# Optimization experiments

Measured on AMD Instinct MI355X. Metric: run time of the kernel, lower is better.

Reference implementation:

```python
import jax, jax.numpy as jnp
import numpy as np

B, S, D, H = 4, 1024, 1024, 16
DK = D // H


def _rel_shift(x):
    # Transformer-XL relative shift: x is (b, h, t1, t2) with t1 == t2
    b, h, t1, t2 = x.shape
    x = jnp.pad(x, ((0, 0), (0, 0), (0, 0), (1, 0)))  # pad left of last dim
    x = x.reshape(b, h, t2 + 1, t1)
    return x[:, :, 1:, :].reshape(b, h, t1, t2)


def setup_inputs() -> dict:
    rng = jax.random.key(0)
    ks = jax.random.split(rng, 10)
    w = 0.02
    return {
        "query": jax.random.normal(ks[0], (B, S, D), jnp.float32),
        "key": jax.random.normal(ks[1], (B, S, D), jnp.float32),
        "value": jax.random.normal(ks[2], (B, S, D), jnp.float32),
        "mask": jnp.ones((B, S), dtype=bool),
        "Wq": jax.random.normal(ks[3], (D, D), jnp.float32) * w,
        "Wk": jax.random.normal(ks[4], (D, D), jnp.float32) * w,
        "Wv": jax.random.normal(ks[5], (D, D), jnp.float32) * w,
        "Wp": jax.random.normal(ks[6], (D, D), jnp.float32) * w,
        "Wo": jax.random.normal(ks[7], (D, D), jnp.float32) * w,
        "pos_bias_u": jax.random.normal(ks[8], (H, DK), jnp.float32) * w,
        "pos_bias_v": jax.random.normal(ks[9], (H, DK), jnp.float32) * w,
    }


def reference(query, key, value, mask, Wq, Wk, Wv, Wp, Wo, pos_bias_u, pos_bias_v):
    b, s, dm = query.shape
    h, dk = pos_bias_u.shape

    # sinusoidal relative position embeddings (positions s-1 ... 0)
    inv_freq = 1.0 / (10000.0 ** (jnp.arange(0, dm, 2, dtype=jnp.float32) / dm))
    pos_seq = jnp.arange(s - 1, -1, -1, dtype=jnp.float32)
    sin_inp = pos_seq[:, None] * inv_freq[None, :]              # (s, dm/2)
    pos_emb = jnp.concatenate([jnp.sin(sin_inp), jnp.cos(sin_inp)], -1)  # (s, dm)

    # projections (torch Linear: y = x @ W.T)
    q = (query @ Wq.T).reshape(b, s, h, dk).transpose(0, 2, 1, 3)  # (b,h,s,dk)
    k = (key @ Wk.T).reshape(b, s, h, dk).transpose(0, 2, 1, 3)
    v = (value @ Wv.T).reshape(b, s, h, dk).transpose(0, 2, 1, 3)
    p = (pos_emb @ Wp.T).reshape(s, h, dk).transpose(1, 0, 2)       # (h,s,dk), same for all batches

    content_score = jnp.einsum('bhqd,bhkd->bhqk', q + pos_bias_u[None, :, None, :], k)
    pos_score = jnp.einsum('bhqd,hkd->bhqk', q + pos_bias_v[None, :, None, :], p)
    pos_score = _rel_shift(pos_score)

    scores = (content_score + pos_score) / jnp.sqrt(jnp.float32(dk))
    attn_mask = mask[:, None, :, None] & mask[:, None, None, :]    # (b,1,q,k)
    scores = jnp.where(attn_mask, scores, jnp.float32(-1e9))

    attn = jax.nn.softmax(scores, axis=-1)  # dropout is identity at eval
    context = jnp.einsum('bhqk,bhkd->bqhd', attn, v).reshape(b, s, dm)
    return context @ Wo.T
```

## Files before the change

### kernel.cpp

```cpp
#include <hip/hip_runtime.h>
#include <math.h>

#define BATCH 4
#define SEQ   1024
#define DM    1024
#define NH    16
#define DK    64

typedef __attribute__((ext_vector_type(8))) short short8;
typedef __attribute__((ext_vector_type(4))) float f32x4;

__device__ inline unsigned short f2bf(float f) {
    unsigned u = __float_as_uint(f);
    unsigned r = (u + 0x7fffu + ((u >> 16) & 1u)) >> 16;
    return (unsigned short)r;
}
__device__ inline float bf2f(unsigned short s) {
    return __uint_as_float(((unsigned)s) << 16);
}
__device__ inline void split1(float x, unsigned short& h, unsigned short& l) {
    h = f2bf(x);
    l = f2bf(x - bf2f(h));
}

__global__ __launch_bounds__(256) void cvt_split(const float4* __restrict__ x,
                                                 ushort4* __restrict__ h,
                                                 ushort4* __restrict__ l, int n4) {
    int i = blockIdx.x * blockDim.x + threadIdx.x;
    if (i >= n4) return;
    float4 v = x[i];
    ushort4 hv, lv;
    split1(v.x, hv.x, lv.x);
    split1(v.y, hv.y, lv.y);
    split1(v.z, hv.z, lv.z);
    split1(v.w, hv.w, lv.w);
    h[i] = hv;
    l[i] = lv;
}

__global__ void posemb_kernel(float* __restrict__ pos_emb) {
    int idx = blockIdx.x * blockDim.x + threadIdx.x;
    if (idx >= SEQ * DM) return;
    int j = idx / DM, d = idx % DM;
    double pos = (double)(SEQ - 1 - j);
    int i = (d < DM / 2) ? d : d - DM / 2;
    double inv_freq = exp(-((2.0 * (double)i) / (double)DM) * log(10000.0));
    double a = pos * inv_freq;
    pos_emb[idx] = (d < DM / 2) ? (float)sin(a) : (float)cos(a);
}

__global__ __launch_bounds__(256) void prep_q(const float4* __restrict__ qp4,
                                              const float4* __restrict__ ub4,
                                              const float4* __restrict__ vb4,
                                              ushort4* __restrict__ quh,
                                              ushort4* __restrict__ qul,
                                              ushort4* __restrict__ qvh,
                                              ushort4* __restrict__ qvl) {
    int i = blockIdx.x * 256 + threadIdx.x;
    float4 q = qp4[i];
    int dm4 = i & (DM / 4 - 1);
    float4 u = ub4[dm4], v = vb4[dm4];
    ushort4 h, l;
    split1(q.x + u.x, h.x, l.x);
    split1(q.y + u.y, h.y, l.y);
    split1(q.z + u.z, h.z, l.z);
    split1(q.w + u.w, h.w, l.w);
    quh[i] = h; qul[i] = l;
    split1(q.x + v.x, h.x, l.x);
    split1(q.y + v.y, h.y, l.y);
    split1(q.z + v.z, h.z, l.z);
    split1(q.w + v.w, h.w, l.w);
    qvh[i] = h; qvl[i] = l;
}

__global__ __launch_bounds__(256) void vtrans_kernel(const float* __restrict__ vp,
                                                     unsigned short* __restrict__ vth,
                                                     unsigned short* __restrict__ vtl) {
    __shared__ float tile[64][65];
    int s0 = blockIdx.x * 64, h = blockIdx.y, b = blockIdx.z;
    int t = threadIdx.x;
#pragma unroll
    for (int i = 0; i < 16; i++) {
        int idx = t + 256 * i;
        int sl = idx >> 6, d = idx & 63;
        tile[sl][d] = vp[((size_t)b * SEQ + s0 + sl) * DM + h * DK + d];
    }
    __syncthreads();
    int bh = b * NH + h;
#pragma unroll
    for (int i = 0; i < 16; i++) {
        int idx = t + 256 * i;
        int dl = idx >> 6, sl = idx & 63;
        float x = tile[sl][dl];
        unsigned short hi, lo;
        split1(x, hi, lo);
        size_t o = ((size_t)bh * DK + dl) * SEQ + s0 + sl;
        vth[o] = hi;
        vtl[o] = lo;
    }
}

__device__ inline void load16(const void* g, void* l) {
    __builtin_amdgcn_global_load_lds(
        (const __attribute__((address_space(1))) unsigned int*)g,
        (__attribute__((address_space(3))) unsigned int*)l, 16, 0, 0);
}

__global__ __launch_bounds__(256) void gemm_split_nt(
        const unsigned short* __restrict__ Ah, const unsigned short* __restrict__ Al,
        const unsigned short* __restrict__ Bh, const unsigned short* __restrict__ Bl,
        float* __restrict__ C, int M, int N, int K,
        long aStride, long bStride, long cStride) {
    __shared__ __attribute__((aligned(16))) short Ah_s[128 * 32];
    __shared__ __attribute__((aligned(16))) short Al_s[128 * 32];
    __shared__ __attribute__((aligned(16))) short Bh_s[128 * 32];
    __shared__ __attribute__((aligned(16))) short Bl_s[128 * 32];

    int z = blockIdx.z;
    Ah += (size_t)z * aStride; Al += (size_t)z * aStride;
    Bh += (size_t)z * bStride; Bl += (size_t)z * bStride;
    C  += (size_t)z * cStride;

    int tid = threadIdx.x, w = tid >> 6, lane = tid & 63;
    int bm = blockIdx.y * 128, bn = blockIdx.x * 128;
    int quad = lane >> 4, tl = lane & 15;
    int wm = (w >> 1) * 64, wn = (w & 1) * 64;

    int sr = w * 32 + (lane >> 2);
    int sc = (lane & 3) * 8;
    const unsigned short* gA0h = Ah + (size_t)(bm + sr) * K + sc;
    const unsigned short* gA1h = Ah + (size_t)(bm + sr + 16) * K + sc;
    const unsigned short* gA0l = Al + (size_t)(bm + sr) * K + sc;
    const unsigned short* gA1l = Al + (size_t)(bm + sr + 16) * K + sc;
    const unsigned short* gB0h = Bh + (size_t)(bn + sr) * K + sc;
    const unsigned short* gB1h = Bh + (size_t)(bn + sr + 16) * K + sc;
    const unsigned short* gB0l = Bl + (size_t)(bn + sr) * K + sc;
    const unsigned short* gB1l = Bl + (size_t)(bn + sr + 16) * K + sc;
    short* lA0h = Ah_s + (w * 32) * 32;  short* lA1h = lA0h + 16 * 32;
    short* lA0l = Al_s + (w * 32) * 32;  short* lA1l = lA0l + 16 * 32;
    short* lB0h = Bh_s + (w * 32) * 32;  short* lB1h = lB0h + 16 * 32;
    short* lB0l = Bl_s + (w * 32) * 32;  short* lB1l = lB0l + 16 * 32;

    f32x4 acc[4][4];
#pragma unroll
    for (int mi = 0; mi < 4; mi++)
#pragma unroll
        for (int ni = 0; ni < 4; ni++)
            acc[mi][ni] = (f32x4){0.f, 0.f, 0.f, 0.f};

    for (int k0 = 0; k0 < K; k0 += 32) {
        load16(gA0h, lA0h); load16(gA1h, lA1h);
        load16(gA0l, lA0l); load16(gA1l, lA1l);
        load16(gB0h, lB0h); load16(gB1h, lB1h);
        load16(gB0l, lB0l); load16(gB1l, lB1l);
        gA0h += 32; gA1h += 32; gA0l += 32; gA1l += 32;
        gB0h += 32; gB1h += 32; gB0l += 32; gB1l += 32;
        __syncthreads();

        short8 ah[4], al[4], bh[4], bl[4];
#pragma unroll
        for (int mi = 0; mi < 4; mi++) {
            int r = wm + mi * 16 + tl;
            ah[mi] = *(const short8*)(Ah_s + r * 32 + quad * 8);
            al[mi] = *(const short8*)(Al_s + r * 32 + quad * 8);
        }
#pragma unroll
        for (int ni = 0; ni < 4; ni++) {
            int r = wn + ni * 16 + tl;
            bh[ni] = *(const short8*)(Bh_s + r * 32 + quad * 8);
            bl[ni] = *(const short8*)(Bl_s + r * 32 + quad * 8);
        }
#pragma unroll
        for (int mi = 0; mi < 4; mi++)
#pragma unroll
            for (int ni = 0; ni < 4; ni++) {
                acc[mi][ni] = __builtin_amdgcn_mfma_f32_16x16x32_bf16(
                    ah[mi], bh[ni], acc[mi][ni], 0, 0, 0);
                acc[mi][ni] = __builtin_amdgcn_mfma_f32_16x16x32_bf16(
                    al[mi], bh[ni], acc[mi][ni], 0, 0, 0);
                acc[mi][ni] = __builtin_amdgcn_mfma_f32_16x16x32_bf16(
                    ah[mi], bl[ni], acc[mi][ni], 0, 0, 0);
            }
        __syncthreads();
    }
#pragma unroll
    for (int mi = 0; mi < 4; mi++)
#pragma unroll
        for (int ni = 0; ni < 4; ni++)
#pragma unroll
            for (int r = 0; r < 4; r++)
                C[(size_t)(bm + wm + mi * 16 + quad * 4 + r) * N +
                  bn + wn + ni * 16 + tl] = acc[mi][ni][r];
}

__global__ __launch_bounds__(256) void gemm_scores(
        const unsigned short* __restrict__ quh, const unsigned short* __restrict__ qul,
        const unsigned short* __restrict__ qvh, const unsigned short* __restrict__ qvl,
        const unsigned short* __restrict__ kh,  const unsigned short* __restrict__ kl,
        const unsigned short* __restrict__ ph,  const unsigned short* __restrict__ pl,
        unsigned short* __restrict__ contC, unsigned short* __restrict__ posC,
        int bh0, int nc) {
    __shared__ __attribute__((aligned(16))) short Ah_s[128 * 32];
    __shared__ __attribute__((aligned(16))) short Al_s[128 * 32];
    __shared__ __attribute__((aligned(16))) short Bh_s[128 * 32];
    __shared__ __attribute__((aligned(16))) short Bl_s[128 * 32];

    int z = blockIdx.z;
    bool isPos = z >= nc;
    int zi = isPos ? z - nc : z;
    int bh = bh0 + zi, b = bh >> 4, h = bh & 15;
    size_t qoff = (size_t)b * SEQ * DM + h * DK;
    const unsigned short *Ah, *Al, *Bh, *Bl;
    if (!isPos) { Ah = quh + qoff; Al = qul + qoff; Bh = kh + qoff; Bl = kl + qoff; }
    else        { Ah = qvh + qoff; Al = qvl + qoff; Bh = ph + h * DK; Bl = pl + h * DK; }
    unsigned short* C = (isPos ? posC : contC) + (size_t)zi * SEQ * SEQ;

    int tid = threadIdx.x, w = tid >> 6, lane = tid & 63;
    int bm = blockIdx.y * 128, bn = blockIdx.x * 128;
    int quad = lane >> 4, tl = lane & 15;
    int wm = (w >> 1) * 64, wn = (w & 1) * 64;

    int sr = w * 32 + (lane >> 2);
    int sc = (lane & 3) * 8;
    const unsigned short* gA0h = Ah + (size_t)(bm + sr) * DM + sc;
    const unsigned short* gA1h = Ah + (size_t)(bm + sr + 16) * DM + sc;
    const unsigned short* gA0l = Al + (size_t)(bm + sr) * DM + sc;
    const unsigned short* gA1l = Al + (size_t)(bm + sr + 16) * DM + sc;
    const unsigned short* gB0h = Bh + (size_t)(bn + sr) * DM + sc;
    const unsigned short* gB1h = Bh + (size_t)(bn + sr + 16) * DM + sc;
    const unsigned short* gB0l = Bl + (size_t)(bn + sr) * DM + sc;
    const unsigned short* gB1l = Bl + (size_t)(bn + sr + 16) * DM + sc;
    short* lA0h = Ah_s + (w * 32) * 32;  short* lA1h = lA0h + 16 * 32;
    short* lA0l = Al_s + (w * 32) * 32;  short* lA1l = lA0l + 16 * 32;
    short* lB0h = Bh_s + (w * 32) * 32;  short* lB1h = lB0h + 16 * 32;
    short* lB0l = Bl_s + (w * 32) * 32;  short* lB1l = lB0l + 16 * 32;

    f32x4 acc[4][4];
#pragma unroll
    for (int mi = 0; mi < 4; mi++)
#pragma unroll
        for (int ni = 0; ni < 4; ni++)
            acc[mi][ni] = (f32x4){0.f, 0.f, 0.f, 0.f};

    for (int k0 = 0; k0 < DK; k0 += 32) {
        load16(gA0h, lA0h); load16(gA1h, lA1h);
        load16(gA0l, lA0l); load16(gA1l, lA1l);
        load16(gB0h, lB0h); load16(gB1h, lB1h);
        load16(gB0l, lB0l); load16(gB1l, lB1l);
        gA0h += 32; gA1h += 32; gA0l += 32; gA1l += 32;
        gB0h += 32; gB1h += 32; gB0l += 32; gB1l += 32;
        __syncthreads();

        short8 ah[4], al[4], bh[4], bl[4];
#pragma unroll
        for (int mi = 0; mi < 4; mi++) {
            int r = wm + mi * 16 + tl;
            ah[mi] = *(const short8*)(Ah_s + r * 32 + quad * 8);
            al[mi] = *(const short8*)(Al_s + r * 32 + quad * 8);
        }
#pragma unroll
        for (int ni = 0; ni < 4; ni++) {
            int r = wn + ni * 16 + tl;
            bh[ni] = *(const short8*)(Bh_s + r * 32 + quad * 8);
            bl[ni] = *(const short8*)(Bl_s + r * 32 + quad * 8);
        }
#pragma unroll
        for (int mi = 0; mi < 4; mi++)
#pragma unroll
            for (int ni = 0; ni < 4; ni++) {
                acc[mi][ni] = __builtin_amdgcn_mfma_f32_16x16x32_bf16(
                    ah[mi], bh[ni], acc[mi][ni], 0, 0, 0);
                acc[mi][ni] = __builtin_amdgcn_mfma_f32_16x16x32_bf16(
                    al[mi], bh[ni], acc[mi][ni], 0, 0, 0);
                acc[mi][ni] = __builtin_amdgcn_mfma_f32_16x16x32_bf16(
                    ah[mi], bl[ni], acc[mi][ni], 0, 0, 0);
            }
        __syncthreads();
    }
#pragma unroll
    for (int mi = 0; mi < 4; mi++)
#pragma unroll
        for (int ni = 0; ni < 4; ni++)
#pragma unroll
            for (int r = 0; r < 4; r++)
                C[(size_t)(bm + wm + mi * 16 + quad * 4 + r) * SEQ +
                  bn + wn + ni * 16 + tl] = f2bf(acc[mi][ni][r]);
}

__global__ __launch_bounds__(512) void content_softmax(
        const unsigned short* __restrict__ quh, const unsigned short* __restrict__ qul,
        const unsigned short* __restrict__ kh,  const unsigned short* __restrict__ kl,
        const unsigned short* __restrict__ posC, unsigned short* __restrict__ contC,
        int bh0) {
    __shared__ __attribute__((aligned(16))) short smem[69632];
    short* S_s = smem + 36864;

    int zi = blockIdx.y;
    int q0 = blockIdx.x * 32;
    int bh = bh0 + zi, b = bh >> 4, h = bh & 15;
    size_t qoff = (size_t)b * SEQ * DM + h * DK;
    const unsigned short* Ah = quh + qoff;
    const unsigned short* Al = qul + qoff;
    const unsigned short* Bh = kh + qoff;
    const unsigned short* Bl = kl + qoff;

    int t = threadIdx.x, w = t >> 6, lane = t & 63;
    int quad = lane >> 4, tl = lane & 15;
    int mi = w >> 2;
    int ni0 = (w & 3) * 2;

    {
        int r8 = w & 3;
        short* dst = smem + (w < 4 ? 0 : 2048) + r8 * 512;
        const unsigned short* srcb = (w < 4 ? Ah : Al);
        load16(srcb + (size_t)(q0 + r8 * 8 + (lane >> 3)) * DM + (lane & 7) * 8, dst);
    }
    {
        int bb = 4096;
#pragma unroll
        for (int i = 0; i < 2; i++) {
            int row = w * 16 + i * 8 + (lane >> 3);
            load16(Bh + (size_t)row * DM + (lane & 7) * 8, smem + bb + w * 1024 + i * 512);
            load16(Bl + (size_t)row * DM + (lane & 7) * 8, smem + bb + 8192 + w * 1024 + i * 512);
        }
    }
    __syncthreads();

    short8 afh[2], afl[2];
#pragma unroll
    for (int kc = 0; kc < 2; kc++) {
        afh[kc] = *(const short8*)(smem + (mi * 16 + tl) * 64 + kc * 32 + quad * 8);
        afl[kc] = *(const short8*)(smem + 2048 + (mi * 16 + tl) * 64 + kc * 32 + quad * 8);
    }

    for (int nb = 0; nb < 8; nb++) {
        int bb  = (nb & 1) ? 20480 : 4096;
        int nbb = (nb & 1) ? 4096 : 20480;
        if (nb < 7) {
            int n0 = (nb + 1) * 128;
#pragma unroll
            for (int i = 0; i < 2; i++) {
                int row = n0 + w * 16 + i * 8 + (lane >> 3);
                load16(Bh + (size_t)row * DM + (lane & 7) * 8, smem + nbb + w * 1024 + i * 512);
                load16(Bl + (size_t)row * DM + (lane & 7) * 8, smem + nbb + 8192 + w * 1024 + i * 512);
            }
        }

        f32x4 acc0 = (f32x4){0.f, 0.f, 0.f, 0.f};
        f32x4 acc1 = (f32x4){0.f, 0.f, 0.f, 0.f};
#pragma unroll
        for (int kc = 0; kc < 2; kc++) {
            short8 bh0f = *(const short8*)(smem + bb + ((ni0) * 16 + tl) * 64 + kc * 32 + quad * 8);
            short8 bl0f = *(const short8*)(smem + bb + 8192 + ((ni0) * 16 + tl) * 64 + kc * 32 + quad * 8);
            short8 bh1f = *(const short8*)(smem + bb + ((ni0 + 1) * 16 + tl) * 64 + kc * 32 + quad * 8);
            short8 bl1f = *(const short8*)(smem + bb + 8192 + ((ni0 + 1) * 16 + tl) * 64 + kc * 32 + quad * 8);
            acc0 = __builtin_amdgcn_mfma_f32_16x16x32_bf16(afh[kc], bh0f, acc0, 0, 0, 0);
            acc0 = __builtin_amdgcn_mfma_f32_16x16x32_bf16(afl[kc], bh0f, acc0, 0, 0, 0);
            acc0 = __builtin_amdgcn_mfma_f32_16x16x32_bf16(afh[kc], bl0f, acc0, 0, 0, 0);
            acc1 = __builtin_amdgcn_mfma_f32_16x16x32_bf16(afh[kc], bh1f, acc1, 0, 0, 0);
            acc1 = __builtin_amdgcn_mfma_f32_16x16x32_bf16(afl[kc], bh1f, acc1, 0, 0, 0);
            acc1 = __builtin_amdgcn_mfma_f32_16x16x32_bf16(afh[kc], bl1f, acc1, 0, 0, 0);
        }
#pragma unroll
        for (int r = 0; r < 4; r++) {
            int row = mi * 16 + quad * 4 + r;
            S_s[row * 1024 + nb * 128 + ni0 * 16 + tl]       = (short)f2bf(acc0[r]);
            S_s[row * 1024 + nb * 128 + (ni0 + 1) * 16 + tl] = (short)f2bf(acc1[r]);
        }
        __syncthreads();
    }

    int nrows = (q0 <= 991) ? 33 : 32;
    {
        float4* P4 = (float4*)smem;
        const float4* src4 = (const float4*)(posC + ((size_t)zi * SEQ + q0) * SEQ);
        int n4 = nrows * 128;
        for (int i = t; i < n4; i += 512) P4[i] = src4[i];
    }
    __syncthreads();

    const unsigned short* P_s = (const unsigned short*)smem;
#pragma unroll
    for (int j = 0; j < 4; j++) {
        int rl = w * 4 + j;
        int q = q0 + rl;
        const short* Srow = S_s + rl * 1024;
        float v[16];
        float m = -1e30f;
#pragma unroll
        for (int s = 0; s < 4; s++) {
            int kb = s * 256 + lane * 4;
            ushort4 sc = *(const ushort4*)(Srow + kb);
#pragma unroll
            for (int e = 0; e < 4; e++) {
                int k = kb + e;
                bool lo = (k <= q);
                int srow = rl + (lo ? 0 : 1);
                int scol = lo ? (k + SEQ - 1 - q) : (k - q - 2);
                float pos = 0.f;
                if (k != q + 1) pos = bf2f(P_s[srow * 1024 + scol]);
                float val = (bf2f(((const unsigned short*)&sc)[e]) + pos) * 0.125f;
                v[s * 4 + e] = val;
                m = fmaxf(m, val);
            }
        }
#pragma unroll
        for (int off = 32; off > 0; off >>= 1) m = fmaxf(m, __shfl_xor(m, off));
        float sum = 0.f;
#pragma unroll
        for (int i = 0; i < 16; i++) { v[i] = __expf(v[i] - m); sum += v[i]; }
#pragma unroll
        for (int off = 32; off > 0; off >>= 1) sum += __shfl_xor(sum, off);
        float inv = 1.0f / sum;
        unsigned short* crow = contC + ((size_t)zi * SEQ + q) * SEQ;
#pragma unroll
        for (int s = 0; s < 4; s++) {
            ushort4 o;
            o.x = f2bf(v[s * 4 + 0] * inv);
            o.y = f2bf(v[s * 4 + 1] * inv);
            o.z = f2bf(v[s * 4 + 2] * inv);
            o.w = f2bf(v[s * 4 + 3] * inv);
            *(ushort4*)(crow + s * 256 + lane * 4) = o;
        }
    }
}

__global__ __launch_bounds__(256) void gemm_pv(
        const unsigned short* __restrict__ probs,
        const unsigned short* __restrict__ vth, const unsigned short* __restrict__ vtl,
        unsigned short* __restrict__ cxh, unsigned short* __restrict__ cxl, int bh0) {
    __shared__ __attribute__((aligned(16))) short As[64 * 64];
    __shared__ __attribute__((aligned(16))) short Bhs[64 * 64];
    __shared__ __attribute__((aligned(16))) short Bls[64 * 64];

    int zi = blockIdx.z;
    int bh = bh0 + zi, b = bh >> 4, h = bh & 15;
    const unsigned short* A  = probs + (size_t)zi * SEQ * SEQ;
    const unsigned short* Bh = vth + (size_t)bh * DK * SEQ;
    const unsigned short* Bl = vtl + (size_t)bh * DK * SEQ;
    size_t coff = (size_t)b * SEQ * DM + h * DK;
    int bm = blockIdx.y * 64;

    int tid = threadIdx.x, w = tid >> 6, lane = tid & 63;
    int quad = lane >> 4, tl = lane & 15;
    int wm = (w >> 1) * 32, wn = (w & 1) * 32;

    int srow = w * 8 + (lane >> 3);
    int scol = (lane & 7) * 8;
    const unsigned short* gA  = A  + (size_t)(bm + srow) * SEQ + scol;
    const unsigned short* gBh = Bh + (size_t)srow * SEQ + scol;
    const unsigned short* gBl = Bl + (size_t)srow * SEQ + scol;

    f32x4 acc[2][2];
#pragma unroll
    for (int mi = 0; mi < 2; mi++)
#pragma unroll
        for (int ni = 0; ni < 2; ni++)
            acc[mi][ni] = (f32x4){0.f, 0.f, 0.f, 0.f};

    for (int k0 = 0; k0 < SEQ; k0 += 64) {
#pragma unroll
        for (int i = 0; i < 2; i++) {
            size_t go = (size_t)i * 32 * SEQ;
            load16(gA + go,  As  + i * 2048 + w * 512);
            load16(gBh + go, Bhs + i * 2048 + w * 512);
            load16(gBl + go, Bls + i * 2048 + w * 512);
        }
        gA += 64; gBh += 64; gBl += 64;
        __syncthreads();

#pragma unroll
        for (int kc = 0; kc < 2; kc++) {
            short8 a[2], bhf[2], blf[2];
#pragma unroll
            for (int mi = 0; mi < 2; mi++)
                a[mi] = *(const short8*)(As + (wm + mi * 16 + tl) * 64 + kc * 32 + quad * 8);
#pragma unroll
            for (int ni = 0; ni < 2; ni++) {
                bhf[ni] = *(const short8*)(Bhs + (wn + ni * 16 + tl) * 64 + kc * 32 + quad * 8);
                blf[ni] = *(const short8*)(Bls + (wn + ni * 16 + tl) * 64 + kc * 32 + quad * 8);
            }
#pragma unroll
            for (int mi = 0; mi < 2; mi++)
#pragma unroll
                for (int ni = 0; ni < 2; ni++) {
                    acc[mi][ni] = __builtin_amdgcn_mfma_f32_16x16x32_bf16(
                        a[mi], bhf[ni], acc[mi][ni], 0, 0, 0);
                    acc[mi][ni] = __builtin_amdgcn_mfma_f32_16x16x32_bf16(
                        a[mi], blf[ni], acc[mi][ni], 0, 0, 0);
                }
        }
        __syncthreads();
    }
#pragma unroll
    for (int mi = 0; mi < 2; mi++)
#pragma unroll
        for (int ni = 0; ni < 2; ni++)
#pragma unroll
            for (int r = 0; r < 4; r++) {
                size_t a = coff +
                    (size_t)(bm + wm + mi * 16 + quad * 4 + r) * DM +
                    wn + ni * 16 + tl;
                unsigned short hh, ll;
                split1(acc[mi][ni][r], hh, ll);
                cxh[a] = hh;
                cxl[a] = ll;
            }
}

extern "C" void kernel_launch(void* const* d_in, const int* in_sizes, int n_in,
                              void* d_out, int out_size, void* d_ws, size_t ws_size,
                              hipStream_t stream) {
    const float* query = (const float*)d_in[0];
    const float* key   = (const float*)d_in[1];
    const float* value = (const float*)d_in[2];
    const float* Wq = (const float*)d_in[4];
    const float* Wk = (const float*)d_in[5];
    const float* Wv = (const float*)d_in[6];
    const float* Wp = (const float*)d_in[7];
    const float* Wo = (const float*)d_in[8];
    const float* pu = (const float*)d_in[9];
    const float* pvb = (const float*)d_in[10];
    float* out = (float*)d_out;

    const size_t MB = 1u << 20;
    char* wsb = (char*)d_ws;
    float* posemb = (float*)(wsb + 0 * MB);
    float* pp     = (float*)(wsb + 4 * MB);
    float* qp     = (float*)(wsb + 8 * MB);
    float* kp     = (float*)(wsb + 24 * MB);
    float* vp     = (float*)(wsb + 40 * MB);
    unsigned short* qAh = (unsigned short*)(wsb + 56 * MB);
    unsigned short* qAl = (unsigned short*)(wsb + 64 * MB);
    unsigned short* kAh = (unsigned short*)(wsb + 72 * MB);
    unsigned short* kAl = (unsigned short*)(wsb + 80 * MB);
    unsigned short* vAh = (unsigned short*)(wsb + 88 * MB);
    unsigned short* vAl = (unsigned short*)(wsb + 96 * MB);
    unsigned short* Wqh = (unsigned short*)(wsb + 104 * MB);
    unsigned short* Wql = (unsigned short*)(wsb + 106 * MB);
    unsigned short* Wkh = (unsigned short*)(wsb + 108 * MB);
    unsigned short* Wkl = (unsigned short*)(wsb + 110 * MB);
    unsigned short* Wvh = (unsigned short*)(wsb + 112 * MB);
    unsigned short* Wvl = (unsigned short*)(wsb + 114 * MB);
    unsigned short* PEh = (unsigned short*)(wsb + 56 * MB);
    unsigned short* PEl = (unsigned short*)(wsb + 58 * MB);
    unsigned short* Wph = (unsigned short*)(wsb + 60 * MB);
    unsigned short* Wpl = (unsigned short*)(wsb + 62 * MB);
    unsigned short* quh = (unsigned short*)(wsb + 56 * MB);
    unsigned short* qul = (unsigned short*)(wsb + 64 * MB);
    unsigned short* qvh = (unsigned short*)(wsb + 72 * MB);
    unsigned short* qvl = (unsigned short*)(wsb + 80 * MB);
    unsigned short* khs = (unsigned short*)(wsb + 88 * MB);
    unsigned short* kls = (unsigned short*)(wsb + 96 * MB);
    unsigned short* phs = (unsigned short*)(wsb + 104 * MB);
    unsigned short* pls = (unsigned short*)(wsb + 106 * MB);
    unsigned short* vth = (unsigned short*)(wsb + 108 * MB);
    unsigned short* vtl = (unsigned short*)(wsb + 116 * MB);
    unsigned short* CXh = (unsigned short*)(wsb + 24 * MB);
    unsigned short* CXl = (unsigned short*)(wsb + 32 * MB);
    unsigned short* Woh = (unsigned short*)(wsb + 40 * MB);
    unsigned short* Wol = (unsigned short*)(wsb + 42 * MB);
    unsigned short* contC = (unsigned short*)(wsb + 124 * MB);

    int nc = (ws_size >= 252 * MB) ? 32 : 16;
    unsigned short* posC = contC + (size_t)nc * SEQ * SEQ;

    const int N4BIG = (BATCH * SEQ * DM) / 4;
    const int N4W   = (DM * DM) / 4;

    posemb_kernel<<<(SEQ * DM + 255) / 256, 256, 0, stream>>>(posemb);

    cvt_split<<<N4BIG / 256, 256, 0, stream>>>((const float4*)query, (ushort4*)qAh, (ushort4*)qAl, N4BIG);
    cvt_split<<<N4BIG / 256, 256, 0, stream>>>((const float4*)key,   (ushort4*)kAh, (ushort4*)kAl, N4BIG);
    cvt_split<<<N4BIG / 256, 256, 0, stream>>>((const float4*)value, (ushort4*)vAh, (ushort4*)vAl, N4BIG);
    cvt_split<<<N4W / 256, 256, 0, stream>>>((const float4*)Wq, (ushort4*)Wqh, (ushort4*)Wql, N4W);
    cvt_split<<<N4W / 256, 256, 0, stream>>>((const float4*)Wk, (ushort4*)Wkh, (ushort4*)Wkl, N4W);
    cvt_split<<<N4W / 256, 256, 0, stream>>>((const float4*)Wv, (ushort4*)Wvh, (ushort4*)Wvl, N4W);
    long aS = 8L * MB, bS = 2L * MB, cS = 4L * MB;
    gemm_split_nt<<<dim3(DM / 128, (BATCH * SEQ) / 128, 3), 256, 0, stream>>>(
        qAh, qAl, Wqh, Wql, qp, BATCH * SEQ, DM, DM, aS, bS, cS);

    cvt_split<<<(SEQ * DM / 4) / 256, 256, 0, stream>>>((const float4*)posemb, (ushort4*)PEh, (ushort4*)PEl, SEQ * DM / 4);
    cvt_split<<<N4W / 256, 256, 0, stream>>>((const float4*)Wp, (ushort4*)Wph, (ushort4*)Wpl, N4W);
    gemm_split_nt<<<dim3(DM / 128, SEQ / 128, 1), 256, 0, stream>>>(
        PEh, PEl, Wph, Wpl, pp, SEQ, DM, DM, 0, 0, 0);

    prep_q<<<N4BIG / 256, 256, 0, stream>>>((const float4*)qp, (const float4*)pu,
                                            (const float4*)pvb, (ushort4*)quh,
                                            (ushort4*)qul, (ushort4*)qvh, (ushort4*)qvl);
    cvt_split<<<N4BIG / 256, 256, 0, stream>>>((const float4*)kp, (ushort4*)khs, (ushort4*)kls, N4BIG);
    cvt_split<<<(SEQ * DM / 4) / 256, 256, 0, stream>>>((const float4*)pp, (ushort4*)phs, (ushort4*)pls, SEQ * DM / 4);
    vtrans_kernel<<<dim3(SEQ / 64, NH, BATCH), 256, 0, stream>>>(vp, vth, vtl);
    cvt_split<<<N4W / 256, 256, 0, stream>>>((const float4*)Wo, (ushort4*)Woh, (ushort4*)Wol, N4W);

    for (int c = 0; c < BATCH * NH; c += nc) {
        gemm_scores<<<dim3(SEQ / 128, SEQ / 128, nc), 256, 0, stream>>>(
            quh, qul, qvh, qvl, khs, kls, phs, pls, contC, posC, c, 0);
        content_softmax<<<dim3(SEQ / 32, nc), 512, 0, stream>>>(
            quh, qul, khs, kls, posC, contC, c);
        gemm_pv<<<dim3(1, SEQ / 64, nc), 256, 0, stream>>>(contC, vth, vtl,
                                                           CXh, CXl, c);
    }

    gemm_split_nt<<<dim3(DM / 128, (BATCH * SEQ) / 128, 1), 256, 0, stream>>>(
        CXh, CXl, Woh, Wol, out, BATCH * SEQ, DM, DM, 0, 0, 0);
}
```

Measured before the change: 607.5 us.

## Fuse PV matmul into softmax kernel and batch pos-proj GEMM with QKV

The softmax kernel now keeps normalized probabilities in shared memory (row stride padded to 1032) and multiplies them directly by V hi/lo fragments loaded from global. This removes the separate gemm_pv kernel and the round trip of the full probability matrix through global memory. The positional-embedding kernel now emits bf16 hi/lo splits directly, and the Wp projection runs as a fourth z-slice of the QKV GEMM launch, dropping a launch and a conversion pass. V is read from global without LDS staging in the fused loop, and each block redoes the V reads, which may add latency. Workspace layout is reshuffled and the contC buffer is removed.

```diff
diff --git a/kernel.cpp b/kernel.cpp
--- a/kernel.cpp
+++ b/kernel.cpp
@@ -38,7 +38,8 @@
     l[i] = lv;
 }
 
-__global__ void posemb_kernel(float* __restrict__ pos_emb) {
+__global__ void posemb_kernel(unsigned short* __restrict__ peh,
+                              unsigned short* __restrict__ pel) {
     int idx = blockIdx.x * blockDim.x + threadIdx.x;
     if (idx >= SEQ * DM) return;
     int j = idx / DM, d = idx % DM;
@@ -46,7 +47,11 @@
     int i = (d < DM / 2) ? d : d - DM / 2;
     double inv_freq = exp(-((2.0 * (double)i) / (double)DM) * log(10000.0));
     double a = pos * inv_freq;
-    pos_emb[idx] = (d < DM / 2) ? (float)sin(a) : (float)cos(a);
+    float v = (d < DM / 2) ? (float)sin(a) : (float)cos(a);
+    unsigned short hh, ll;
+    split1(v, hh, ll);
+    peh[idx] = hh;
+    pel[idx] = ll;
 }
 
 __global__ __launch_bounds__(256) void prep_q(const float4* __restrict__ qp4,
@@ -110,19 +115,27 @@
         const unsigned short* __restrict__ Ah, const unsigned short* __restrict__ Al,
         const unsigned short* __restrict__ Bh, const unsigned short* __restrict__ Bl,
         float* __restrict__ C, int M, int N, int K,
-        long aStride, long bStride, long cStride) {
+        long aStride, long bStride, long cStride,
+        const unsigned short* __restrict__ PEh, const unsigned short* __restrict__ PEl,
+        const unsigned short* __restrict__ Wph, const unsigned short* __restrict__ Wpl,
+        float* __restrict__ Cp) {
     __shared__ __attribute__((aligned(16))) short Ah_s[128 * 32];
     __shared__ __attribute__((aligned(16))) short Al_s[128 * 32];
     __shared__ __attribute__((aligned(16))) short Bh_s[128 * 32];
     __shared__ __attribute__((aligned(16))) short Bl_s[128 * 32];
 
     int z = blockIdx.z;
-    Ah += (size_t)z * aStride; Al += (size_t)z * aStride;
-    Bh += (size_t)z * bStride; Bl += (size_t)z * bStride;
-    C  += (size_t)z * cStride;
+    int bm = blockIdx.y * 128, bn = blockIdx.x * 128;
+    if (z == 3) {
+        if (bm >= SEQ) return;
+        Ah = PEh; Al = PEl; Bh = Wph; Bl = Wpl; C = Cp;
+    } else {
+        Ah += (size_t)z * aStride; Al += (size_t)z * aStride;
+        Bh += (size_t)z * bStride; Bl += (size_t)z * bStride;
+        C  += (size_t)z * cStride;
+    }
 
     int tid = threadIdx.x, w = tid >> 6, lane = tid & 63;
-    int bm = blockIdx.y * 128, bn = blockIdx.x * 128;
     int quad = lane >> 4, tl = lane & 15;
     int wm = (w >> 1) * 64, wn = (w & 1) * 64;
 
@@ -290,9 +303,11 @@
 __global__ __launch_bounds__(512) void content_softmax(
         const unsigned short* __restrict__ quh, const unsigned short* __restrict__ qul,
         const unsigned short* __restrict__ kh,  const unsigned short* __restrict__ kl,
-        const unsigned short* __restrict__ posC, unsigned short* __restrict__ contC,
+        const unsigned short* __restrict__ posC,
+        const unsigned short* __restrict__ vth, const unsigned short* __restrict__ vtl,
+        unsigned short* __restrict__ cxh, unsigned short* __restrict__ cxl,
         int bh0) {
-    __shared__ __attribute__((aligned(16))) short smem[69632];
+    __shared__ __attribute__((aligned(16))) short smem[69888];
     short* S_s = smem + 36864;
 
     int zi = blockIdx.y;
@@ -364,8 +379,8 @@
 #pragma unroll
         for (int r = 0; r < 4; r++) {
             int row = mi * 16 + quad * 4 + r;
-            S_s[row * 1024 + nb * 128 + ni0 * 16 + tl]       = (short)f2bf(acc0[r]);
-            S_s[row * 1024 + nb * 128 + (ni0 + 1) * 16 + tl] = (short)f2bf(acc1[r]);
+            S_s[row * 1032 + nb * 128 + ni0 * 16 + tl]       = (short)f2bf(acc0[r]);
+            S_s[row * 1032 + nb * 128 + (ni0 + 1) * 16 + tl] = (short)f2bf(acc1[r]);
         }
         __syncthreads();
     }
@@ -384,7 +399,7 @@
     for (int j = 0; j < 4; j++) {
         int rl = w * 4 + j;
         int q = q0 + rl;
-        const short* Srow = S_s + rl * 1024;
+        short* Srow = S_s + rl * 1032;
         float v[16];
         float m = -1e30f;
 #pragma unroll
@@ -412,7 +427,6 @@
 #pragma unroll
         for (int off = 32; off > 0; off >>= 1) sum += __shfl_xor(sum, off);
         float inv = 1.0f / sum;
-        unsigned short* crow = contC + ((size_t)zi * SEQ + q) * SEQ;
 #pragma unroll
         for (int s = 0; s < 4; s++) {
             ushort4 o;
@@ -420,92 +434,44 @@
             o.y = f2bf(v[s * 4 + 1] * inv);
             o.z = f2bf(v[s * 4 + 2] * inv);
             o.w = f2bf(v[s * 4 + 3] * inv);
-            *(ushort4*)(crow + s * 256 + lane * 4) = o;
-        }
-    }
-}
-
-__global__ __launch_bounds__(256) void gemm_pv(
-        const unsigned short* __restrict__ probs,
-        const unsigned short* __restrict__ vth, const unsigned short* __restrict__ vtl,
-        unsigned short* __restrict__ cxh, unsigned short* __restrict__ cxl, int bh0) {
-    __shared__ __attribute__((aligned(16))) short As[64 * 64];
-    __shared__ __attribute__((aligned(16))) short Bhs[64 * 64];
-    __shared__ __attribute__((aligned(16))) short Bls[64 * 64];
-
-    int zi = blockIdx.z;
-    int bh = bh0 + zi, b = bh >> 4, h = bh & 15;
-    const unsigned short* A  = probs + (size_t)zi * SEQ * SEQ;
-    const unsigned short* Bh = vth + (size_t)bh * DK * SEQ;
-    const unsigned short* Bl = vtl + (size_t)bh * DK * SEQ;
-    size_t coff = (size_t)b * SEQ * DM + h * DK;
-    int bm = blockIdx.y * 64;
-
-    int tid = threadIdx.x, w = tid >> 6, lane = tid & 63;
-    int quad = lane >> 4, tl = lane & 15;
-    int wm = (w >> 1) * 32, wn = (w & 1) * 32;
-
-    int srow = w * 8 + (lane >> 3);
-    int scol = (lane & 7) * 8;
-    const unsigned short* gA  = A  + (size_t)(bm + srow) * SEQ + scol;
-    const unsigned short* gBh = Bh + (size_t)srow * SEQ + scol;
-    const unsigned short* gBl = Bl + (size_t)srow * SEQ + scol;
-
-    f32x4 acc[2][2];
-#pragma unroll
-    for (int mi = 0; mi < 2; mi++)
-#pragma unroll
-        for (int ni = 0; ni < 2; ni++)
-            acc[mi][ni] = (f32x4){0.f, 0.f, 0.f, 0.f};
-
-    for (int k0 = 0; k0 < SEQ; k0 += 64) {
-#pragma unroll
-        for (int i = 0; i < 2; i++) {
-            size_t go = (size_t)i * 32 * SEQ;
-            load16(gA + go,  As  + i * 2048 + w * 512);
-            load16(gBh + go, Bhs + i * 2048 + w * 512);
-            load16(gBl + go, Bls + i * 2048 + w * 512);
-        }
-        gA += 64; gBh += 64; gBl += 64;
-        __syncthreads();
-
-#pragma unroll
-        for (int kc = 0; kc < 2; kc++) {
-            short8 a[2], bhf[2], blf[2];
-#pragma unroll
-            for (int mi = 0; mi < 2; mi++)
-                a[mi] = *(const short8*)(As + (wm + mi * 16 + tl) * 64 + kc * 32 + quad * 8);
-#pragma unroll
-            for (int ni = 0; ni < 2; ni++) {
-                bhf[ni] = *(const short8*)(Bhs + (wn + ni * 16 + tl) * 64 + kc * 32 + quad * 8);
-                blf[ni] = *(const short8*)(Bls + (wn + ni * 16 + tl) * 64 + kc * 32 + quad * 8);
+            *(ushort4*)((unsigned short*)Srow + s * 256 + lane * 4) = o;
+        }
+    }
+    __syncthreads();
+
+    {
+        int niw = w & 3;
+        const unsigned short* gVh = vth + ((size_t)bh * DK + niw * 16 + tl) * SEQ + quad * 8;
+        const unsigned short* gVl = vtl + ((size_t)bh * DK + niw * 16 + tl) * SEQ + quad * 8;
+        const short* As0 = S_s + (mi * 16 + tl) * 1032 + quad * 8;
+        f32x4 p0 = (f32x4){0.f, 0.f, 0.f, 0.f};
+        f32x4 p1 = (f32x4){0.f, 0.f, 0.f, 0.f};
+        for (int nb = 0; nb < 8; nb++) {
+#pragma unroll
+            for (int kc = 0; kc < 4; kc++) {
+                int ko = nb * 128 + kc * 32;
+                short8 a   = *(const short8*)(As0 + ko);
+                short8 vh8 = *(const short8*)(gVh + ko);
+                short8 vl8 = *(const short8*)(gVl + ko);
+                if (kc & 1) {
+                    p1 = __builtin_amdgcn_mfma_f32_16x16x32_bf16(a, vh8, p1, 0, 0, 0);
+                    p1 = __builtin_amdgcn_mfma_f32_16x16x32_bf16(a, vl8, p1, 0, 0, 0);
+                } else {
+                    p0 = __builtin_amdgcn_mfma_f32_16x16x32_bf16(a, vh8, p0, 0, 0, 0);
+                    p0 = __builtin_amdgcn_mfma_f32_16x16x32_bf16(a, vl8, p0, 0, 0, 0);
+                }
             }
-#pragma unroll
-            for (int mi = 0; mi < 2; mi++)
-#pragma unroll
-                for (int ni = 0; ni < 2; ni++) {
-                    acc[mi][ni] = __builtin_amdgcn_mfma_f32_16x16x32_bf16(
-                        a[mi], bhf[ni], acc[mi][ni], 0, 0, 0);
-                    acc[mi][ni] = __builtin_amdgcn_mfma_f32_16x16x32_bf16(
-                        a[mi], blf[ni], acc[mi][ni], 0, 0, 0);
-                }
-        }
-        __syncthreads();
-    }
-#pragma unroll
-    for (int mi = 0; mi < 2; mi++)
-#pragma unroll
-        for (int ni = 0; ni < 2; ni++)
-#pragma unroll
-            for (int r = 0; r < 4; r++) {
-                size_t a = coff +
-                    (size_t)(bm + wm + mi * 16 + quad * 4 + r) * DM +
-                    wn + ni * 16 + tl;
-                unsigned short hh, ll;
-                split1(acc[mi][ni][r], hh, ll);
-                cxh[a] = hh;
-                cxl[a] = ll;
-            }
+        }
+#pragma unroll
+        for (int r = 0; r < 4; r++) {
+            float val = p0[r] + p1[r];
+            size_t a = qoff + (size_t)(q0 + mi * 16 + quad * 4 + r) * DM + niw * 16 + tl;
+            unsigned short hh, ll;
+            split1(val, hh, ll);
+            cxh[a] = hh;
+            cxl[a] = ll;
+        }
+    }
 }
 
 extern "C" void kernel_launch(void* const* d_in, const int* in_sizes, int n_in,
@@ -525,7 +491,6 @@
 
     const size_t MB = 1u << 20;
     char* wsb = (char*)d_ws;
-    float* posemb = (float*)(wsb + 0 * MB);
     float* pp     = (float*)(wsb + 4 * MB);
     float* qp     = (float*)(wsb + 8 * MB);
     float* kp     = (float*)(wsb + 24 * MB);
@@ -542,10 +507,10 @@
     unsigned short* Wkl = (unsigned short*)(wsb + 110 * MB);
     unsigned short* Wvh = (unsigned short*)(wsb + 112 * MB);
     unsigned short* Wvl = (unsigned short*)(wsb + 114 * MB);
-    unsigned short* PEh = (unsigned short*)(wsb + 56 * MB);
-    unsigned short* PEl = (unsigned short*)(wsb + 58 * MB);
-    unsigned short* Wph = (unsigned short*)(wsb + 60 * MB);
-    unsigned short* Wpl = (unsigned short*)(wsb + 62 * MB);
+    unsigned short* PEh = (unsigned short*)(wsb + 116 * MB);
+    unsigned short* PEl = (unsigned short*)(wsb + 118 * MB);
+    unsigned short* Wph = (unsigned short*)(wsb + 120 * MB);
+    unsigned short* Wpl = (unsigned short*)(wsb + 122 * MB);
     unsigned short* quh = (unsigned short*)(wsb + 56 * MB);
     unsigned short* qul = (unsigned short*)(wsb + 64 * MB);
     unsigned short* qvh = (unsigned short*)(wsb + 72 * MB);
@@ -560,15 +525,15 @@
     unsigned short* CXl = (unsigned short*)(wsb + 32 * MB);
     unsigned short* Woh = (unsigned short*)(wsb + 40 * MB);
     unsigned short* Wol = (unsigned short*)(wsb + 42 * MB);
-    unsigned short* contC = (unsigned short*)(wsb + 124 * MB);
-
-    int nc = (ws_size >= 252 * MB) ? 32 : 16;
-    unsigned short* posC = contC + (size_t)nc * SEQ * SEQ;
+    unsigned short* posC = (unsigned short*)(wsb + 124 * MB);
+
+    int nc = (ws_size >= 188 * MB) ? 32 : 16;
 
     const int N4BIG = (BATCH * SEQ * DM) / 4;
     const int N4W   = (DM * DM) / 4;
 
-    posemb_kernel<<<(SEQ * DM + 255) / 256, 256, 0, stream>>>(posemb);
+    posemb_kernel<<<(SEQ * DM + 255) / 256, 256, 0, stream>>>(PEh, PEl);
+    cvt_split<<<N4W / 256, 256, 0, stream>>>((const float4*)Wp, (ushort4*)Wph, (ushort4*)Wpl, N4W);
 
     cvt_split<<<N4BIG / 256, 256, 0, stream>>>((const float4*)query, (ushort4*)qAh, (ushort4*)qAl, N4BIG);
     cvt_split<<<N4BIG / 256, 256, 0, stream>>>((const float4*)key,   (ushort4*)kAh, (ushort4*)kAl, N4BIG);
@@ -577,13 +542,9 @@
     cvt_split<<<N4W / 256, 256, 0, stream>>>((const float4*)Wk, (ushort4*)Wkh, (ushort4*)Wkl, N4W);
     cvt_split<<<N4W / 256, 256, 0, stream>>>((const float4*)Wv, (ushort4*)Wvh, (ushort4*)Wvl, N4W);
     long aS = 8L * MB, bS = 2L * MB, cS = 4L * MB;
-    gemm_split_nt<<<dim3(DM / 128, (BATCH * SEQ) / 128, 3), 256, 0, stream>>>(
-        qAh, qAl, Wqh, Wql, qp, BATCH * SEQ, DM, DM, aS, bS, cS);
-
-    cvt_split<<<(SEQ * DM / 4) / 256, 256, 0, stream>>>((const float4*)posemb, (ushort4*)PEh, (ushort4*)PEl, SEQ * DM / 4);
-    cvt_split<<<N4W / 256, 256, 0, stream>>>((const float4*)Wp, (ushort4*)Wph, (ushort4*)Wpl, N4W);
-    gemm_split_nt<<<dim3(DM / 128, SEQ / 128, 1), 256, 0, stream>>>(
-        PEh, PEl, Wph, Wpl, pp, SEQ, DM, DM, 0, 0, 0);
+    gemm_split_nt<<<dim3(DM / 128, (BATCH * SEQ) / 128, 4), 256, 0, stream>>>(
+        qAh, qAl, Wqh, Wql, qp, BATCH * SEQ, DM, DM, aS, bS, cS,
+        PEh, PEl, Wph, Wpl, pp);
 
     prep_q<<<N4BIG / 256, 256, 0, stream>>>((const float4*)qp, (const float4*)pu,
                                             (const float4*)pvb, (ushort4*)quh,
@@ -595,13 +556,12 @@
 
     for (int c = 0; c < BATCH * NH; c += nc) {
         gemm_scores<<<dim3(SEQ / 128, SEQ / 128, nc), 256, 0, stream>>>(
-            quh, qul, qvh, qvl, khs, kls, phs, pls, contC, posC, c, 0);
+            quh, qul, qvh, qvl, khs, kls, phs, pls, posC, posC, c, 0);
         content_softmax<<<dim3(SEQ / 32, nc), 512, 0, stream>>>(
-            quh, qul, khs, kls, posC, contC, c);
-        gemm_pv<<<dim3(1, SEQ / 64, nc), 256, 0, stream>>>(contC, vth, vtl,
-                                                           CXh, CXl, c);
+            quh, qul, khs, kls, posC, vth, vtl, CXh, CXl, c);
     }
 
     gemm_split_nt<<<dim3(DM / 128, (BATCH * SEQ) / 128, 1), 256, 0, stream>>>(
-        CXh, CXl, Woh, Wol, out, BATCH * SEQ, DM, DM, 0, 0, 0);
-}
+        CXh, CXl, Woh, Wol, out, BATCH * SEQ, DM, DM, 0, 0, 0,
+        nullptr, nullptr, nullptr, nullptr, nullptr);
+}
```

New measurement: 642.6 us. 1.06x slower.
